# Optimization experiments

Measured on AMD Instinct MI355X. Metric: run time of the kernel, lower is better.

## Reference

```python
import jax, jax.numpy as jnp
import numpy as np

B, Z, L = 256, 256, 8
C0, H0, W0 = 128, 8, 8
O = C0 * H0 * W0  # 8192


def _conv_transpose(x, w, b):
    """Torch ConvTranspose2d(k=4, s=2, p=1) equivalent.
    w: torch layout (in_ch, out_ch, kH, kW).
    Implemented as lhs-dilated conv with flipped, transposed kernel; pad = k-1-p = 2.
    """
    wt = jnp.flip(w, (2, 3)).transpose(1, 0, 2, 3)  # (out, in, kh, kw)
    y = jax.lax.conv_general_dilated(
        x, wt, window_strides=(1, 1), padding=[(2, 2), (2, 2)],
        lhs_dilation=(2, 2), dimension_numbers=('NCHW', 'OIHW', 'NCHW'))
    return y + b[None, :, None, None]


def setup_inputs() -> dict:
    key = jax.random.key(0)
    ks = jax.random.split(key, 6)
    return {
        'x': jax.random.normal(ks[0], (B, Z), jnp.float32),
        'gw': jax.random.normal(ks[1], (Z, L), jnp.float32) * (2.0 / (Z + L)) ** 0.5,  # xavier_normal
        'gb': jnp.zeros((L,), jnp.float32),
        'pw': jax.random.normal(ks[2], (O, Z, L), jnp.float32) * (1.0 / Z) ** 0.5,  # kaiming linear
        'pb': jnp.zeros((O, L), jnp.float32),
        'w1': jax.random.normal(ks[3], (C0, 64, 4, 4), jnp.float32) * 0.02,
        'b1': jnp.zeros((64,), jnp.float32),
        'w2': jax.random.normal(ks[4], (64, 32, 4, 4), jnp.float32) * 0.02,
        'b2': jnp.zeros((32,), jnp.float32),
        'w3': jax.random.normal(ks[5], (32, 3, 4, 4), jnp.float32) * 0.02,
        'b3': jnp.zeros((3,), jnp.float32),
    }


def reference(x, gw, gb, pw, pb, w1, b1, w2, b2, w3, b3):
    # --- ME mixture of linear experts (linear projection) ---
    g = jax.nn.softmax(x @ gw + gb, axis=1)               # (B, L)
    # Per-expert linear outputs, then gate-weighted sum. Mathematically equal to
    # torch's (pw @ gatings) per-sample weight followed by bmm with x, but avoids
    # the (B, O, Z) intermediate.
    expert_out = jnp.einsum('bi,oil->bol', x, pw)          # (B, O, L)
    out = jnp.einsum('bol,bl->bo', expert_out, g) + g @ pb.T  # (B, O)
    # --- conv-transpose decoder stack ---
    h = out.reshape(B, C0, H0, W0)
    h = jax.nn.relu(_conv_transpose(h, w1, b1))            # (B, 64, 16, 16)
    h = jax.nn.relu(_conv_transpose(h, w2, b2))            # (B, 32, 32, 32)
    h = _conv_transpose(h, w3, b3)                         # (B, 3, 64, 64)
    return h
```

## Files before the change

kernel.cpp:

```cpp
#include <hip/hip_runtime.h>

typedef __bf16 bf16;
typedef __bf16 bf16x8 __attribute__((ext_vector_type(8)));
typedef float f32x4 __attribute__((ext_vector_type(4)));

__device__ __forceinline__ f32x4 mfma16(bf16x8 a, bf16x8 b, f32x4 c) {
  return __builtin_amdgcn_mfma_f32_16x16x32_bf16(a, b, c, 0, 0, 0);
}

__device__ __forceinline__ void gload16(const void* g, void* l) {
  __builtin_amdgcn_global_load_lds(
      (const __attribute__((address_space(1))) void*)g,
      (__attribute__((address_space(3))) void*)(uint32_t)(size_t)l, 16, 0, 0);
}

__device__ __forceinline__ bf16x8 cvt8(float4 a, float4 b) {
  bf16x8 r;
  r[0] = (bf16)a.x; r[1] = (bf16)a.y; r[2] = (bf16)a.z; r[3] = (bf16)a.w;
  r[4] = (bf16)b.x; r[5] = (bf16)b.y; r[6] = (bf16)b.z; r[7] = (bf16)b.w;
  return r;
}

__global__ __launch_bounds__(256) void gating_kernel(
    const float* __restrict__ x, const float* __restrict__ gw,
    const float* __restrict__ gb, bf16* __restrict__ xgb,
    float* __restrict__ gbuf) {
  const int b = blockIdx.x, tid = threadIdx.x;
  __shared__ float xs[256];
  __shared__ float gs[8];
  xs[tid] = x[b * 256 + tid];
  __syncthreads();
  if (tid < 8) {
    float acc = gb[tid];
    for (int i = 0; i < 256; ++i) acc += xs[i] * gw[i * 8 + tid];
    gs[tid] = acc;
  }
  __syncthreads();
  if (tid == 0) {
    float m = gs[0];
    for (int l = 1; l < 8; ++l) m = fmaxf(m, gs[l]);
    float s = 0.f, e[8];
    for (int l = 0; l < 8; ++l) { e[l] = expf(gs[l] - m); s += e[l]; }
    float inv = 1.f / s;
    for (int l = 0; l < 8; ++l) gs[l] = e[l] * inv;
  }
  __syncthreads();
  if (tid < 8) gbuf[b * 8 + tid] = gs[tid];
  bf16* dst = xgb + (size_t)b * 2048;
  for (int k = tid; k < 2048; k += 256)
    dst[k] = (bf16)(xs[k >> 3] * gs[k & 7]);
}

template <int CIN, int COUT, int COUTP>
__device__ __forceinline__ void cw_one(const float* __restrict__ w,
                                       bf16* __restrict__ wp, int idx) {
  constexpr int K = 4 * CIN;
  int ic = idx & (CIN - 1);
  int t = (idx / CIN) & 3;
  int oc = (idx / K) % COUTP;
  int p = idx / (K * COUTP);
  bf16 v = (bf16)0.f;
  if (oc < COUT) {
    int py = p >> 1, px = p & 1, tyi = t >> 1, txi = t & 1;
    int ky = py == 0 ? (tyi ? 3 : 1) : (tyi ? 2 : 0);
    int kx = px == 0 ? (txi ? 3 : 1) : (txi ? 2 : 0);
    v = (bf16)w[((ic * COUT + oc) * 4 + ky) * 4 + kx];
  }
  wp[idx] = v;
}

__global__ __launch_bounds__(256) void convert_w_all(
    const float* __restrict__ w1, bf16* __restrict__ w1p,
    const float* __restrict__ w2, bf16* __restrict__ w2p,
    const float* __restrict__ w3, bf16* __restrict__ w3p) {
  int idx = blockIdx.x * 256 + threadIdx.x;
  if (idx < 131072) cw_one<128, 64, 64>(w1, w1p, idx);
  else if (idx < 163840) cw_one<64, 32, 32>(w2, w2p, idx - 131072);
  else if (idx < 172032) cw_one<32, 3, 16>(w3, w3p, idx - 163840);
}

template <int HP, int WP, int C>
__device__ __forceinline__ void bz_one(bf16* __restrict__ buf, int idx) {
  constexpr int NCELL = 2 * WP + 2 * (HP - 2);
  constexpr int C8 = C / 8;
  int c8 = idx % C8;
  int rem = idx / C8;
  int cell = rem % NCELL;
  int b = rem / NCELL;
  int y, x;
  if (cell < WP) { y = 0; x = cell; }
  else if (cell < 2 * WP) { y = HP - 1; x = cell - WP; }
  else { int r2 = cell - 2 * WP; y = 1 + (r2 >> 1); x = (r2 & 1) ? WP - 1 : 0; }
  bf16x8 z = {};
  *(bf16x8*)(buf + ((size_t)(b * HP + y) * WP + x) * C + c8 * 8) = z;
}

__global__ __launch_bounds__(256) void border_zero_all(
    bf16* __restrict__ h0t, bf16* __restrict__ h1, bf16* __restrict__ h2) {
  int idx = blockIdx.x * 256 + threadIdx.x;
  if (idx < 147456) bz_one<10, 10, 128>(h0t, idx);
  else if (idx < 286720) bz_one<18, 18, 64>(h1, idx - 147456);
  else if (idx < 421888) bz_one<34, 34, 32>(h2, idx - 286720);
}

__global__ __launch_bounds__(256) void me_gemm_kernel(
    const float* __restrict__ pw, const bf16* __restrict__ xgb,
    const float* __restrict__ pb, const float* __restrict__ gbuf,
    bf16* __restrict__ h0t) {
  __shared__ char sB[16384];
  const int tid = threadIdx.x, wv = tid >> 6, l = tid & 63;
  const int lr = l & 15, lkg = l >> 4;
  const int oM0 = (blockIdx.x >> 2) * 64, bN0 = (blockIdx.x & 3) * 64;

  const int r1 = tid >> 3, c1 = tid & 7;
  const int sb1 = (c1 * 16) ^ ((r1 & 7) << 4);
  const int r2 = r1 + 32;
  const int sb2 = (c1 * 16) ^ ((r2 & 7) << 4);
  const bf16* bsrc1 = xgb + (size_t)(bN0 + r1) * 2048 + (sb1 >> 1);
  const bf16* bsrc2 = xgb + (size_t)(bN0 + r2) * 2048 + (sb2 >> 1);
  const int bdst1 = wv * 1024, bdst2 = 4096 + wv * 1024;

  const float* pAf = pw + (size_t)(oM0 + wv * 16 + lr) * 2048 + lkg * 8;

  int raddrB[4][2];
#pragma unroll
  for (int n = 0; n < 4; ++n) {
    int rb = n * 16 + lr;
#pragma unroll
    for (int ks = 0; ks < 2; ++ks)
      raddrB[n][ks] = rb * 128 + ((ks * 64 + lkg * 16) ^ ((rb & 7) << 4));
  }

  gload16(bsrc1, sB + bdst1);
  gload16(bsrc2, sB + bdst2);
  float4 c0 = *(const float4*)(pAf);
  float4 c1f = *(const float4*)(pAf + 4);
  float4 c2 = *(const float4*)(pAf + 32);
  float4 c3 = *(const float4*)(pAf + 36);

  f32x4 acc[4] = {};
  __syncthreads();
  for (int kt = 0; kt < 32; ++kt) {
    const int cur = (kt & 1) * 8192;
    float4 n0, n1, n2, n3;
    if (kt < 31) {
      const int nxt = ((kt + 1) & 1) * 8192;
      const int ke = (kt + 1) * 64;
      gload16(bsrc1 + ke, sB + nxt + bdst1);
      gload16(bsrc2 + ke, sB + nxt + bdst2);
      n0 = *(const float4*)(pAf + ke);
      n1 = *(const float4*)(pAf + ke + 4);
      n2 = *(const float4*)(pAf + ke + 32);
      n3 = *(const float4*)(pAf + ke + 36);
    }
    bf16x8 af0 = cvt8(c0, c1f);
    bf16x8 af1 = cvt8(c2, c3);
#pragma unroll
    for (int ks = 0; ks < 2; ++ks)
#pragma unroll
      for (int n = 0; n < 4; ++n) {
        bf16x8 bv = *(const bf16x8*)(sB + cur + raddrB[n][ks]);
        acc[n] = mfma16(ks ? af1 : af0, bv, acc[n]);
      }
    if (kt < 31) { c0 = n0; c1f = n1; c2 = n2; c3 = n3; }
    __syncthreads();
  }

  float4 g0[4], g1[4];
#pragma unroll
  for (int n = 0; n < 4; ++n) {
    int b = bN0 + n * 16 + lr;
    g0[n] = *(const float4*)(gbuf + b * 8);
    g1[n] = *(const float4*)(gbuf + b * 8 + 4);
  }
#pragma unroll
  for (int r = 0; r < 4; ++r) {
    int o = oM0 + wv * 16 + lkg * 4 + r;
    float4 p0 = *(const float4*)(pb + o * 8);
    float4 p1 = *(const float4*)(pb + o * 8 + 4);
    int cch = o >> 6, y = (o >> 3) & 7, xx = o & 7;
#pragma unroll
    for (int n = 0; n < 4; ++n) {
      int b = bN0 + n * 16 + lr;
      float bias = g0[n].x * p0.x + g0[n].y * p0.y + g0[n].z * p0.z + g0[n].w * p0.w +
                   g1[n].x * p1.x + g1[n].y * p1.y + g1[n].z * p1.z + g1[n].w * p1.w;
      h0t[((size_t)(b * 10 + y + 1) * 10 + xx + 1) * 128 + cch] = (bf16)(acc[n][r] + bias);
    }
  }
}

template <int CIN, int H, int YB, int COUTP, int WM, int NF, int SWM,
          bool WLDS, int INIT, int WIT, bool RELU, bool F32OUT, int SIN_SZ, int SW_SZ>
__global__ __launch_bounds__(256) void convt_kernel(
    const bf16* __restrict__ in, const bf16* __restrict__ wp,
    const float* __restrict__ bias, bf16* __restrict__ out,
    float* __restrict__ fout) {
  constexpr int W = H, WROW = W + 2, ROWB = CIN * 2, GRS = ROWB / 16;
  constexpr int LGR = (GRS == 16) ? 4 : (GRS == 8) ? 3 : 2;
  constexpr int LW = (W == 8) ? 3 : (W == 16) ? 4 : 5;
  constexpr int K = 4 * CIN;
  constexpr int CHUNKS = (YB + 2) * WROW * GRS;
  constexpr int WGR = K / 8;
  __shared__ char sIn[SIN_SZ];
  __shared__ char sW[SW_SZ];

  const int tid = threadIdx.x, wv = tid >> 6, l = tid & 63;
  const int nyb = H / YB;
  const int img = blockIdx.x / nyb, y0 = (blockIdx.x % nyb) * YB;
  const int p = blockIdx.y, py = p >> 1, px = p & 1;

#pragma unroll
  for (int it = 0; it < INIT; ++it) {
    int t = it * 256 + tid;
    int tc = t < CHUNKS ? t : CHUNKS - 1;
    int pix = tc >> LGR, cc = tc & (GRS - 1);
    int ly = pix / WROW, lx = pix % WROW;
    int sb = (cc * 16) ^ ((pix & SWM) << 4);
    gload16(in + ((size_t)((img * (H + 2) + y0 + ly) * (W + 2) + lx)) * CIN + (sb >> 1),
            sIn + it * 4096 + wv * 1024);
  }
  if constexpr (WLDS) {
#pragma unroll
    for (int it = 0; it < WIT; ++it) {
      int t = it * 256 + tid;
      int oc = t / WGR, cc = t % WGR;
      int sb = (cc * 16) ^ ((oc & 7) << 4);
      gload16(wp + (size_t)(p * COUTP + oc) * K + (sb >> 1), sW + it * 4096 + wv * 1024);
    }
  }
  __syncthreads();

  const int lr = l & 15, lkg = l >> 4;
  const int wm = wv & (WM - 1), wn = wv / WM;
  int pcen[2];
#pragma unroll
  for (int m = 0; m < 2; ++m) {
    int r = wm * 32 + m * 16 + lr;
    pcen[m] = ((r >> LW) + 1) * WROW + (r & (W - 1)) + 1;
  }

  f32x4 acc[2][NF] = {};
#pragma unroll 4
  for (int kk = 0; kk < K; kk += 32) {
    const int t4 = kk / CIN;
    const int tyi = t4 >> 1, txi = t4 & 1;
    const int dy = (py == 0) ? (tyi ? -1 : 0) : (tyi ? 0 : 1);
    const int dx = (px == 0) ? (txi ? -1 : 0) : (txi ? 0 : 1);
    const int icb = (kk % CIN) * 2 + lkg * 16;
    bf16x8 av[2], bv[NF];
#pragma unroll
    for (int m = 0; m < 2; ++m) {
      int pixd = pcen[m] + dy * WROW + dx;
      av[m] = *(const bf16x8*)(sIn + pixd * ROWB + (icb ^ ((pixd & SWM) << 4)));
    }
#pragma unroll
    for (int n = 0; n < NF; ++n) {
      int oc = (wn * NF + n) * 16 + lr;
      if constexpr (WLDS) {
        int kb = kk * 2 + lkg * 16;
        bv[n] = *(const bf16x8*)(sW + oc * (K * 2) + (kb ^ ((oc & 7) << 4)));
      } else {
        bv[n] = *(const bf16x8*)(wp + (size_t)(p * COUTP + oc) * K + kk + lkg * 8);
      }
    }
#pragma unroll
    for (int m = 0; m < 2; ++m)
#pragma unroll
      for (int n = 0; n < NF; ++n) acc[m][n] = mfma16(av[m], bv[n], acc[m][n]);
  }

#pragma unroll
  for (int m = 0; m < 2; ++m)
#pragma unroll
    for (int r4 = 0; r4 < 4; ++r4) {
      int r = wm * 32 + m * 16 + lkg * 4 + r4;
      int yy = r >> LW, xx = r & (W - 1);
      int oy = 2 * (y0 + yy) + py, ox = 2 * xx + px;
#pragma unroll
      for (int n = 0; n < NF; ++n) {
        int oc = (wn * NF + n) * 16 + lr;
        float v = acc[m][n][r4];
        if constexpr (F32OUT) {
          if (oc < 3) fout[((size_t)(img * 3 + oc) * (2 * H) + oy) * (2 * H) + ox] = v + bias[oc];
        } else {
          v += bias[oc];
          if constexpr (RELU) v = fmaxf(v, 0.f);
          out[((size_t)(img * (2 * H + 2) + oy + 1) * (2 * H + 2) + ox + 1) * COUTP + oc] = (bf16)v;
        }
      }
    }
}

extern "C" void kernel_launch(void* const* d_in, const int* in_sizes, int n_in,
                              void* d_out, int out_size, void* d_ws, size_t ws_size,
                              hipStream_t stream) {
  const float* x  = (const float*)d_in[0];
  const float* gw = (const float*)d_in[1];
  const float* gb = (const float*)d_in[2];
  const float* pw = (const float*)d_in[3];
  const float* pb = (const float*)d_in[4];
  const float* w1 = (const float*)d_in[5];
  const float* b1 = (const float*)d_in[6];
  const float* w2 = (const float*)d_in[7];
  const float* b2 = (const float*)d_in[8];
  const float* w3 = (const float*)d_in[9];
  const float* b3 = (const float*)d_in[10];
  float* outp = (float*)d_out;

  char* ws = (char*)d_ws;
  bf16*  xgb  = (bf16*)(ws + 0);
  float* gbuf = (float*)(ws + 1048576);
  bf16*  h0t  = (bf16*)(ws + 1056768);
  bf16*  w1p  = (bf16*)(ws + 7610368);
  bf16*  h1   = (bf16*)(ws + 7872512);
  bf16*  w2p  = (bf16*)(ws + 18489344);
  bf16*  h2   = (bf16*)(ws + 18554880);
  bf16*  w3p  = (bf16*)(ws + 37494784);

  border_zero_all<<<1648, 256, 0, stream>>>(h0t, h1, h2);
  gating_kernel<<<256, 256, 0, stream>>>(x, gw, gb, xgb, gbuf);
  convert_w_all<<<672, 256, 0, stream>>>(w1, w1p, w2, w2p, w3, w3p);

  me_gemm_kernel<<<512, 256, 0, stream>>>(pw, xgb, pb, gbuf, h0t);

  convt_kernel<128, 8, 8, 64, 2, 2, 7, false, 7, 0, true, false, 28672, 16>
      <<<dim3(256, 4), 256, 0, stream>>>(h0t, w1p, b1, h1, nullptr);
  convt_kernel<64, 16, 8, 32, 4, 2, 7, true, 6, 4, true, false, 24576, 16384>
      <<<dim3(512, 4), 256, 0, stream>>>(h1, w2p, b2, h2, nullptr);
  convt_kernel<32, 32, 4, 16, 4, 1, 3, true, 4, 1, false, true, 16384, 4096>
      <<<dim3(2048, 4), 256, 0, stream>>>(h2, w3p, b3, nullptr, outp);
}
```

Baseline: 119.2 us.

## Restructure ME GEMM to stage whole A tile in LDS, stream B from global

The ME projection GEMM changes tiling. Each block now converts a full 32-row strip of the fp32 expert weights (all K=2048) to bf16 into 128KB of LDS up front, then its 8 waves each cover 32 batch columns and read the B operand (x times gates) directly from global memory. Each pw element is now read exactly once, with no per-k-tile syncs or double buffering. The trade-off is a large LDS footprint that limits occupancy to one block per CU, no overlap between the A load phase and the MFMA phase, and uncoalesced global B reads.

```diff
diff --git a/kernel.cpp b/kernel.cpp
--- a/kernel.cpp
+++ b/kernel.cpp
@@ -103,90 +103,76 @@
   else if (idx < 421888) bz_one<34, 34, 32>(h2, idx - 286720);
 }
 
-__global__ __launch_bounds__(256) void me_gemm_kernel(
+__global__ __launch_bounds__(512) void me_gemm_kernel(
     const float* __restrict__ pw, const bf16* __restrict__ xgb,
     const float* __restrict__ pb, const float* __restrict__ gbuf,
     bf16* __restrict__ h0t) {
-  __shared__ char sB[16384];
+  __shared__ char sA[131072];
   const int tid = threadIdx.x, wv = tid >> 6, l = tid & 63;
   const int lr = l & 15, lkg = l >> 4;
-  const int oM0 = (blockIdx.x >> 2) * 64, bN0 = (blockIdx.x & 3) * 64;
-
-  const int r1 = tid >> 3, c1 = tid & 7;
-  const int sb1 = (c1 * 16) ^ ((r1 & 7) << 4);
-  const int r2 = r1 + 32;
-  const int sb2 = (c1 * 16) ^ ((r2 & 7) << 4);
-  const bf16* bsrc1 = xgb + (size_t)(bN0 + r1) * 2048 + (sb1 >> 1);
-  const bf16* bsrc2 = xgb + (size_t)(bN0 + r2) * 2048 + (sb2 >> 1);
-  const int bdst1 = wv * 1024, bdst2 = 4096 + wv * 1024;
-
-  const float* pAf = pw + (size_t)(oM0 + wv * 16 + lr) * 2048 + lkg * 8;
-
-  int raddrB[4][2];
-#pragma unroll
-  for (int n = 0; n < 4; ++n) {
-    int rb = n * 16 + lr;
+  const int M0 = blockIdx.x * 32;
+
+#pragma unroll 4
+  for (int it = 0; it < 16; ++it) {
+    int g = it * 512 + tid;
+    int kt = g >> 8, rem = g & 255;
+    int row = rem >> 3, ig = rem & 7;
+    const float* src = pw + (size_t)(M0 + row) * 2048 + kt * 64 + ig * 8;
+    float4 v0 = *(const float4*)src;
+    float4 v1 = *(const float4*)(src + 4);
+    int L = kt * 4096 + row * 128 + ((ig * 16) ^ ((row & 7) << 4));
+    *(bf16x8*)(sA + L) = cvt8(v0, v1);
+  }
+  __syncthreads();
+
+  int aoff[2][2];
+#pragma unroll
+  for (int m = 0; m < 2; ++m)
 #pragma unroll
     for (int ks = 0; ks < 2; ++ks)
-      raddrB[n][ks] = rb * 128 + ((ks * 64 + lkg * 16) ^ ((rb & 7) << 4));
-  }
-
-  gload16(bsrc1, sB + bdst1);
-  gload16(bsrc2, sB + bdst2);
-  float4 c0 = *(const float4*)(pAf);
-  float4 c1f = *(const float4*)(pAf + 4);
-  float4 c2 = *(const float4*)(pAf + 32);
-  float4 c3 = *(const float4*)(pAf + 36);
-
-  f32x4 acc[4] = {};
-  __syncthreads();
-  for (int kt = 0; kt < 32; ++kt) {
-    const int cur = (kt & 1) * 8192;
-    float4 n0, n1, n2, n3;
-    if (kt < 31) {
-      const int nxt = ((kt + 1) & 1) * 8192;
-      const int ke = (kt + 1) * 64;
-      gload16(bsrc1 + ke, sB + nxt + bdst1);
-      gload16(bsrc2 + ke, sB + nxt + bdst2);
-      n0 = *(const float4*)(pAf + ke);
-      n1 = *(const float4*)(pAf + ke + 4);
-      n2 = *(const float4*)(pAf + ke + 32);
-      n3 = *(const float4*)(pAf + ke + 36);
-    }
-    bf16x8 af0 = cvt8(c0, c1f);
-    bf16x8 af1 = cvt8(c2, c3);
-#pragma unroll
-    for (int ks = 0; ks < 2; ++ks)
-#pragma unroll
-      for (int n = 0; n < 4; ++n) {
-        bf16x8 bv = *(const bf16x8*)(sB + cur + raddrB[n][ks]);
-        acc[n] = mfma16(ks ? af1 : af0, bv, acc[n]);
-      }
-    if (kt < 31) { c0 = n0; c1f = n1; c2 = n2; c3 = n3; }
-    __syncthreads();
-  }
-
-  float4 g0[4], g1[4];
-#pragma unroll
-  for (int n = 0; n < 4; ++n) {
-    int b = bN0 + n * 16 + lr;
+      aoff[m][ks] = (m * 16 + lr) * 128 + (((ks * 4 + lkg) * 16) ^ ((lr & 7) << 4));
+
+  const bf16* pB0 = xgb + (size_t)(wv * 32 + lr) * 2048 + lkg * 8;
+  const bf16* pB1 = pB0 + 16 * 2048;
+
+  f32x4 acc[2][2] = {};
+#pragma unroll 4
+  for (int s = 0; s < 64; ++s) {
+    const int kt = s >> 1, ks = s & 1;
+    const char* base = sA + kt * 4096;
+    bf16x8 a0 = *(const bf16x8*)(base + aoff[0][ks]);
+    bf16x8 a1 = *(const bf16x8*)(base + aoff[1][ks]);
+    bf16x8 b0 = *(const bf16x8*)(pB0 + s * 32);
+    bf16x8 b1 = *(const bf16x8*)(pB1 + s * 32);
+    acc[0][0] = mfma16(a0, b0, acc[0][0]);
+    acc[0][1] = mfma16(a0, b1, acc[0][1]);
+    acc[1][0] = mfma16(a1, b0, acc[1][0]);
+    acc[1][1] = mfma16(a1, b1, acc[1][1]);
+  }
+
+  float4 g0[2], g1[2];
+#pragma unroll
+  for (int n = 0; n < 2; ++n) {
+    int b = wv * 32 + n * 16 + lr;
     g0[n] = *(const float4*)(gbuf + b * 8);
     g1[n] = *(const float4*)(gbuf + b * 8 + 4);
   }
 #pragma unroll
-  for (int r = 0; r < 4; ++r) {
-    int o = oM0 + wv * 16 + lkg * 4 + r;
-    float4 p0 = *(const float4*)(pb + o * 8);
-    float4 p1 = *(const float4*)(pb + o * 8 + 4);
-    int cch = o >> 6, y = (o >> 3) & 7, xx = o & 7;
-#pragma unroll
-    for (int n = 0; n < 4; ++n) {
-      int b = bN0 + n * 16 + lr;
-      float bias = g0[n].x * p0.x + g0[n].y * p0.y + g0[n].z * p0.z + g0[n].w * p0.w +
-                   g1[n].x * p1.x + g1[n].y * p1.y + g1[n].z * p1.z + g1[n].w * p1.w;
-      h0t[((size_t)(b * 10 + y + 1) * 10 + xx + 1) * 128 + cch] = (bf16)(acc[n][r] + bias);
-    }
-  }
+  for (int m = 0; m < 2; ++m)
+#pragma unroll
+    for (int r = 0; r < 4; ++r) {
+      int o = M0 + m * 16 + lkg * 4 + r;
+      float4 p0 = *(const float4*)(pb + o * 8);
+      float4 p1 = *(const float4*)(pb + o * 8 + 4);
+      int cch = o >> 6, y = (o >> 3) & 7, xx = o & 7;
+#pragma unroll
+      for (int n = 0; n < 2; ++n) {
+        int b = wv * 32 + n * 16 + lr;
+        float bias = g0[n].x * p0.x + g0[n].y * p0.y + g0[n].z * p0.z + g0[n].w * p0.w +
+                     g1[n].x * p1.x + g1[n].y * p1.y + g1[n].z * p1.z + g1[n].w * p1.w;
+        h0t[((size_t)(b * 10 + y + 1) * 10 + xx + 1) * 128 + cch] = (bf16)(acc[m][n][r] + bias);
+      }
+    }
 }
 
 template <int CIN, int H, int YB, int COUTP, int WM, int NF, int SWM,
@@ -321,7 +307,7 @@
   gating_kernel<<<256, 256, 0, stream>>>(x, gw, gb, xgb, gbuf);
   convert_w_all<<<672, 256, 0, stream>>>(w1, w1p, w2, w2p, w3, w3p);
 
-  me_gemm_kernel<<<512, 256, 0, stream>>>(pw, xgb, pb, gbuf, h0t);
+  me_gemm_kernel<<<256, 512, 0, stream>>>(pw, xgb, pb, gbuf, h0t);
 
   convt_kernel<128, 8, 8, 64, 2, 2, 7, false, 7, 0, true, false, 28672, 16>
       <<<dim3(256, 4), 256, 0, stream>>>(h0t, w1p, b1, h1, nullptr);
```

Result: slower. 130.3 us (+9.4%).
